# Performance work log

Measured on AMD Instinct MI355X. Metric: run time of the kernel, lower is better.

## Reference

```python
import jax, jax.numpy as jnp
import numpy as np

EMB = 512
HEADS = 8
B, T = 4, 1024


def setup_inputs() -> dict:
    key = jax.random.key(0)
    k1, k2, k3, k4, k5 = jax.random.split(key, 5)
    scale = 1.0 / np.sqrt(EMB)
    x = jax.random.normal(k1, (B, T, EMB), dtype=jnp.float32)
    # Linear(emb, emb*heads, bias=False) weights, stored as [in, out] for x @ W
    Wk = jax.random.normal(k2, (EMB, EMB * HEADS), dtype=jnp.float32) * scale
    Wq = jax.random.normal(k3, (EMB, EMB * HEADS), dtype=jnp.float32) * scale
    Wv = jax.random.normal(k4, (EMB, EMB * HEADS), dtype=jnp.float32) * scale
    Wu = jax.random.normal(k5, (EMB * HEADS, EMB), dtype=jnp.float32) * (1.0 / np.sqrt(EMB * HEADS))
    return {"x": x, "Wk": Wk, "Wq": Wq, "Wv": Wv, "Wu": Wu}


def reference(x, Wk, Wq, Wv, Wu):
    b, t, k = x.shape
    h = HEADS
    # projections -> [b, h, t, k]
    keys = (x @ Wk).reshape(b, t, h, k).transpose(0, 2, 1, 3)
    queries = (x @ Wq).reshape(b, t, h, k).transpose(0, 2, 1, 3)
    values = (x @ Wv).reshape(b, t, h, k).transpose(0, 2, 1, 3)
    # NOTE: original computes bmm(keys, queries^T): dot[i,j] = key_i . query_j
    dot = jnp.einsum('bhik,bhjk->bhij', keys, queries)  # [b,h,t,t]
    # mask_fn: only upper-triangle (offset=1) entries that are EXACTLY zero get -inf
    triu = jnp.triu(jnp.ones((t, t), dtype=bool), k=1)
    final_mask = triu & (dot == 0)
    dot = jnp.where(final_mask, -jnp.inf, dot)
    attn = jax.nn.softmax(dot, axis=-1)
    out = jnp.einsum('bhij,bhjk->bhik', attn, values)  # [b,h,t,k]
    out = out.transpose(0, 2, 1, 3).reshape(b, t, h * k)
    return out @ Wu
```

## Files before the change

### kernel.cpp

```cpp
#include <hip/hip_runtime.h>
#include <stdint.h>

typedef _Float16 f16x8 __attribute__((ext_vector_type(8)));
typedef float f32x4 __attribute__((ext_vector_type(4)));

__device__ __forceinline__ unsigned short f2h(float f) {
  _Float16 h = (_Float16)f;
  return __builtin_bit_cast(unsigned short, h);
}

#if __has_builtin(__builtin_amdgcn_global_load_lds)
#define HAVE_GLL 1
__device__ __forceinline__ void gload_lds16(const void* g, void* l) {
  auto gp = reinterpret_cast<const __attribute__((address_space(1))) void*>(
      reinterpret_cast<uintptr_t>(g));
  auto lp = reinterpret_cast<__attribute__((address_space(3))) void*>(
      reinterpret_cast<uintptr_t>(l));
  __builtin_amdgcn_global_load_lds(gp, lp, 16, 0, 0);
}
#else
#define HAVE_GLL 0
#endif

__device__ __forceinline__ void transpose_core(const float* in, unsigned short* out,
                                               int R, int C, int c0, int r0) {
  __shared__ float t[32][33];
  int tx = threadIdx.x & 31, ty = threadIdx.x >> 5;
#pragma unroll
  for (int i = 0; i < 32; i += 8)
    t[ty + i][tx] = in[(long)(r0 + ty + i) * C + (c0 + tx)];
  __syncthreads();
#pragma unroll
  for (int i = 0; i < 32; i += 8)
    out[(long)(c0 + ty + i) * R + (r0 + tx)] = f2h(t[tx][ty + i]);
}

__global__ __launch_bounds__(256) void k_setup(
    const float* __restrict__ x, const float* __restrict__ W0, const float* __restrict__ W1,
    const float* __restrict__ W2, const float* __restrict__ W3,
    unsigned short* __restrict__ Xh, unsigned short* __restrict__ o0,
    unsigned short* __restrict__ o1, unsigned short* __restrict__ o2,
    unsigned short* __restrict__ o3) {
  int z = blockIdx.z;
  if (z == 4) {
    int i = (blockIdx.y * 128 + blockIdx.x) * 256 + threadIdx.x;
    float4 v = reinterpret_cast<const float4*>(x)[i];
    ushort4 o;
    o.x = f2h(v.x); o.y = f2h(v.y); o.z = f2h(v.z); o.w = f2h(v.w);
    reinterpret_cast<ushort4*>(Xh)[i] = o;
  } else if (z < 3) {
    const float* in = (z == 0) ? W0 : (z == 1) ? W1 : W2;
    unsigned short* out = (z == 0) ? o0 : (z == 1) ? o1 : o2;
    transpose_core(in, out, 512, 4096, blockIdx.x * 32, blockIdx.y * 32);
  } else {
    transpose_core(W3, o3, 4096, 512, blockIdx.y * 32, blockIdx.x * 32);
  }
}

template <int OUT>
__device__ __forceinline__ void gemm_core(const unsigned short* __restrict__ A,
                                          const unsigned short* __restrict__ B,
                                          void* __restrict__ Cv, int K, int lda, int ldb,
                                          int ldc, long coff, int m0, int n0) {
  __shared__ unsigned short As[128 * 64];
  __shared__ unsigned short Bs[128 * 64];

  int tid = threadIdx.x;
  int wid = tid >> 6, lane = tid & 63;
  int wm = (wid >> 1) * 64, wn = (wid & 1) * 64;
  int rq = lane >> 4, rl = lane & 15;

  f32x4 acc[4][4];
#pragma unroll
  for (int i = 0; i < 4; ++i)
#pragma unroll
    for (int j = 0; j < 4; ++j) acc[i][j] = (f32x4){0.f, 0.f, 0.f, 0.f};

#if HAVE_GLL
  int cg = (lane & 7) ^ ((lane >> 3) & 7);
  int rl8 = lane >> 3;
#endif

  for (int k0 = 0; k0 < K; k0 += 64) {
    __syncthreads();
#if HAVE_GLL
#pragma unroll
    for (int t = 0; t < 4; ++t) {
      int r = wid * 32 + t * 8;
      gload_lds16(&A[(long)(m0 + r + rl8) * lda + k0 + cg * 8], &As[r * 64]);
      gload_lds16(&B[(long)(n0 + r + rl8) * ldb + k0 + cg * 8], &Bs[r * 64]);
    }
#else
#pragma unroll
    for (int it = 0; it < 4; ++it) {
      int idx = tid + it * 256;
      int r = idx >> 3, c = idx & 7;
      int cs = c ^ (r & 7);
      *reinterpret_cast<uint4*>(&As[r * 64 + cs * 8]) =
          *reinterpret_cast<const uint4*>(&A[(long)(m0 + r) * lda + k0 + c * 8]);
      *reinterpret_cast<uint4*>(&Bs[r * 64 + cs * 8]) =
          *reinterpret_cast<const uint4*>(&B[(long)(n0 + r) * ldb + k0 + c * 8]);
    }
#endif
    __syncthreads();
#pragma unroll
    for (int ks = 0; ks < 2; ++ks) {
      f16x8 af[4], bfr[4];
      int kc = ks * 4 + rq;
#pragma unroll
      for (int i = 0; i < 4; ++i) {
        int ra = wm + i * 16 + rl;
        af[i] = *reinterpret_cast<const f16x8*>(&As[ra * 64 + ((kc ^ (ra & 7)) << 3)]);
        int rb = wn + i * 16 + rl;
        bfr[i] = *reinterpret_cast<const f16x8*>(&Bs[rb * 64 + ((kc ^ (rb & 7)) << 3)]);
      }
#pragma unroll
      for (int i = 0; i < 4; ++i)
#pragma unroll
        for (int j = 0; j < 4; ++j)
          acc[i][j] = __builtin_amdgcn_mfma_f32_16x16x32_f16(af[i], bfr[j], acc[i][j], 0, 0, 0);
    }
  }

#pragma unroll
  for (int i = 0; i < 4; ++i)
#pragma unroll
    for (int j = 0; j < 4; ++j)
#pragma unroll
      for (int r = 0; r < 4; ++r) {
        long row = m0 + wm + i * 16 + rq * 4 + r;
        long col = n0 + wn + j * 16 + rl;
        float v = acc[i][j][r];
        if (OUT == 1)
          reinterpret_cast<unsigned short*>(Cv)[coff + row * ldc + col] = f2h(v);
        else if (OUT == 0)
          reinterpret_cast<float*>(Cv)[coff + row * ldc + col] = v;
        else
          atomicAdd(&reinterpret_cast<float*>(Cv)[coff + row * ldc + col], v);
      }
}

template <int OUT>
__global__ __launch_bounds__(256, 2) void k_gemm_btx(
    const unsigned short* __restrict__ A, const unsigned short* __restrict__ B,
    void* __restrict__ Cv, int K, int lda, int ldb, int ldc,
    long oAo, long oAi, long oBo, long oBi, long oCo, long oCi, int zdiv,
    int sx, int sy) {
  int c = blockIdx.x, w = blockIdx.y;
  int z = c + 8 * (w >> (sx + sy));
  int y = (w >> sx) & ((1 << sy) - 1);
  int x = w & ((1 << sx) - 1);
  A += (long)(z / zdiv) * oAo + (long)(z % zdiv) * oAi;
  B += (long)(z / zdiv) * oBo + (long)(z % zdiv) * oBi;
  long coff = (long)(z / zdiv) * oCo + (long)(z % zdiv) * oCi;
  gemm_core<OUT>(A, B, Cv, K, lda, ldb, ldc, coff, y * 128, x * 128);
}

__global__ __launch_bounds__(256, 2) void k_gemm_qkv(
    const unsigned short* __restrict__ X, const unsigned short* __restrict__ Wqt,
    const unsigned short* __restrict__ Wkt, const unsigned short* __restrict__ Wvt,
    unsigned short* __restrict__ Qb, unsigned short* __restrict__ Kb,
    unsigned short* __restrict__ Vt) {
  int z = blockIdx.z;
  const unsigned short* A = (z == 2) ? Wvt : X;
  const unsigned short* B = (z == 0) ? Wqt : (z == 1) ? Wkt : X;
  unsigned short* C = (z == 0) ? Qb : (z == 1) ? Kb : Vt;
  gemm_core<1>(A, B, C, 512, 512, 512, 4096, 0, blockIdx.y * 128, blockIdx.x * 128);
}

__global__ __launch_bounds__(256, 2) void k_gemm_splitk(
    const unsigned short* __restrict__ A, const unsigned short* __restrict__ B,
    float* __restrict__ C, int lda, int ldb, int ldc) {
  int c = blockIdx.x, w = blockIdx.y;
  int g = c + 8 * (w >> 2);
  int y = g & 31, z = g >> 5, x = w & 3;
  gemm_core<2>(A + (long)z * 1024, B + (long)z * 1024, C, 1024, lda, ldb, ldc, 0,
               y * 128, x * 128);
}

__global__ __launch_bounds__(256) void k_softmax_w(unsigned short* __restrict__ S) {
  long row = (long)blockIdx.x * 4 + (threadIdx.x >> 6);
  int lane = threadIdx.x & 63;
  f16x8* p = reinterpret_cast<f16x8*>(S + row * 1024);
  f16x8 a = p[lane * 2], b = p[lane * 2 + 1];
  float v[16];
#pragma unroll
  for (int i = 0; i < 8; ++i) { v[i] = (float)a[i]; v[8 + i] = (float)b[i]; }
  float m = v[0];
#pragma unroll
  for (int i = 1; i < 16; ++i) m = fmaxf(m, v[i]);
#pragma unroll
  for (int o = 32; o; o >>= 1) m = fmaxf(m, __shfl_xor(m, o));
  float s = 0.f;
#pragma unroll
  for (int i = 0; i < 16; ++i) { v[i] = __expf(v[i] - m); s += v[i]; }
#pragma unroll
  for (int o = 32; o; o >>= 1) s += __shfl_xor(s, o);
  float inv = 1.0f / s;
  f16x8 oa, ob;
#pragma unroll
  for (int i = 0; i < 8; ++i) {
    oa[i] = (_Float16)(v[i] * inv);
    ob[i] = (_Float16)(v[8 + i] * inv);
  }
  p[lane * 2] = oa;
  p[lane * 2 + 1] = ob;
}

__global__ void k_sentinel(float* out, float v) { out[0] = v; }

extern "C" void kernel_launch(void* const* d_in, const int* in_sizes, int n_in,
                              void* d_out, int out_size, void* d_ws, size_t ws_size,
                              hipStream_t stream) {
  const float* x  = (const float*)d_in[0];
  const float* Wk = (const float*)d_in[1];
  const float* Wq = (const float*)d_in[2];
  const float* Wv = (const float*)d_in[3];
  const float* Wu = (const float*)d_in[4];
  float* out = (float*)d_out;

  const long SZ_X = 4096L * 512;
  const long SZ_W = 512L * 4096;
  const size_t NEED = 188743680;

  if (ws_size < NEED) {
    hipMemsetAsync(d_out, 0, (size_t)out_size * 4, stream);
    k_sentinel<<<1, 1, 0, stream>>>(out, (float)ws_size);
    return;
  }

  char* p = (char*)d_ws;
  unsigned short* Xbf = (unsigned short*)p; p += SZ_X * 2;
  unsigned short* Wqt = (unsigned short*)p; p += SZ_W * 2;
  unsigned short* Wkt = (unsigned short*)p; p += SZ_W * 2;
  unsigned short* Wvt = (unsigned short*)p; p += SZ_W * 2;
  unsigned short* Wut = (unsigned short*)p; p += SZ_W * 2;
  unsigned short* Qb = (unsigned short*)p; p += 4096L * 4096 * 2;
  unsigned short* Kb = (unsigned short*)p; p += 4096L * 4096 * 2;
  unsigned short* Vt = (unsigned short*)p; p += 4096L * 4096 * 2;
  unsigned short* S16 = (unsigned short*)p;
  unsigned short* Ob = Qb;

  hipMemsetAsync(d_out, 0, (size_t)out_size * 4, stream);

  k_setup<<<dim3(128, 16, 5), 256, 0, stream>>>(x, Wq, Wk, Wv, Wu, Xbf, Wqt, Wkt, Wvt, Wut);

  k_gemm_qkv<<<dim3(32, 32, 3), 256, 0, stream>>>(Xbf, Wqt, Wkt, Wvt, Qb, Kb, Vt);

  k_gemm_btx<1><<<dim3(8, 256), 256, 0, stream>>>(
      Kb, Qb, S16, 512, 4096, 4096, 1024,
      4194304, 512, 4194304, 512, 8388608, 1048576, 8, 3, 3);
  k_softmax_w<<<8192, 256, 0, stream>>>(S16);
  k_gemm_btx<1><<<dim3(8, 128), 256, 0, stream>>>(
      S16, Vt, Ob, 1024, 1024, 4096, 4096,
      8388608, 1048576, 1024, 2097152, 4194304, 512, 8, 2, 3);

  k_gemm_splitk<<<dim3(8, 64), 256, 0, stream>>>(Ob, Wut, out, 4096, 4096, 512);
}
```

Baseline: 284.3 us.

## Fold Wv into Wu to fuse value and output projections

Precomputes per-head Wv·Wu products so values are projected directly into the output space, giving VU of width 512 per head. The PV matmul and the final output projection then collapse into a single split-K GEMM that accumulates atomically into the output. Scores are written in an interleaved layout so the new softmax and the fused GEMM can read P as one wide matrix. This removes the large [4096x4096] O intermediate and one GEMM, but adds a small weight-product GEMM, changes the fp16 rounding path, and relies on atomics across heads.

```diff
diff --git a/kernel.cpp b/kernel.cpp
--- a/kernel.cpp
+++ b/kernel.cpp
@@ -36,24 +36,26 @@
 }
 
 __global__ __launch_bounds__(256) void k_setup(
-    const float* __restrict__ x, const float* __restrict__ W0, const float* __restrict__ W1,
-    const float* __restrict__ W2, const float* __restrict__ W3,
-    unsigned short* __restrict__ Xh, unsigned short* __restrict__ o0,
-    unsigned short* __restrict__ o1, unsigned short* __restrict__ o2,
-    unsigned short* __restrict__ o3) {
+    const float* __restrict__ x, const float* __restrict__ Wq, const float* __restrict__ Wk,
+    const float* __restrict__ Wv, const float* __restrict__ Wu,
+    unsigned short* __restrict__ Xh, unsigned short* __restrict__ Wqt,
+    unsigned short* __restrict__ Wkt, unsigned short* __restrict__ Wvh,
+    unsigned short* __restrict__ Wut) {
   int z = blockIdx.z;
-  if (z == 4) {
+  if (z == 0) {
+    transpose_core(Wq, Wqt, 512, 4096, blockIdx.x * 32, blockIdx.y * 32);
+  } else if (z == 1) {
+    transpose_core(Wk, Wkt, 512, 4096, blockIdx.x * 32, blockIdx.y * 32);
+  } else if (z == 2) {
+    transpose_core(Wu, Wut, 4096, 512, blockIdx.y * 32, blockIdx.x * 32);
+  } else {
+    const float* in = (z == 3) ? x : Wv;
+    unsigned short* out = (z == 3) ? Xh : Wvh;
     int i = (blockIdx.y * 128 + blockIdx.x) * 256 + threadIdx.x;
-    float4 v = reinterpret_cast<const float4*>(x)[i];
+    float4 v = reinterpret_cast<const float4*>(in)[i];
     ushort4 o;
     o.x = f2h(v.x); o.y = f2h(v.y); o.z = f2h(v.z); o.w = f2h(v.w);
-    reinterpret_cast<ushort4*>(Xh)[i] = o;
-  } else if (z < 3) {
-    const float* in = (z == 0) ? W0 : (z == 1) ? W1 : W2;
-    unsigned short* out = (z == 0) ? o0 : (z == 1) ? o1 : o2;
-    transpose_core(in, out, 512, 4096, blockIdx.x * 32, blockIdx.y * 32);
-  } else {
-    transpose_core(W3, o3, 4096, 512, blockIdx.y * 32, blockIdx.x * 32);
+    reinterpret_cast<ushort4*>(out)[i] = o;
   }
 }
 
@@ -128,15 +130,20 @@
     for (int j = 0; j < 4; ++j)
 #pragma unroll
       for (int r = 0; r < 4; ++r) {
-        long row = m0 + wm + i * 16 + rq * 4 + r;
-        long col = n0 + wn + j * 16 + rl;
+        int row = m0 + wm + i * 16 + rq * 4 + r;
+        int col = n0 + wn + j * 16 + rl;
         float v = acc[i][j][r];
         if (OUT == 1)
-          reinterpret_cast<unsigned short*>(Cv)[coff + row * ldc + col] = f2h(v);
+          reinterpret_cast<unsigned short*>(Cv)[coff + (long)row * ldc + col] = f2h(v);
         else if (OUT == 0)
-          reinterpret_cast<float*>(Cv)[coff + row * ldc + col] = v;
-        else
-          atomicAdd(&reinterpret_cast<float*>(Cv)[coff + row * ldc + col], v);
+          reinterpret_cast<float*>(Cv)[coff + (long)row * ldc + col] = v;
+        else if (OUT == 2)
+          atomicAdd(&reinterpret_cast<float*>(Cv)[coff + (long)row * ldc + col], v);
+        else {
+          long addr = (long)(col >> 10) * 4194304 + (long)(row & 511) * 8192 +
+                      ((row >> 9) << 10) + (col & 1023);
+          reinterpret_cast<unsigned short*>(Cv)[addr] = f2h(v);
+        }
       }
 }
 
@@ -158,50 +165,48 @@
 
 __global__ __launch_bounds__(256, 2) void k_gemm_qkv(
     const unsigned short* __restrict__ X, const unsigned short* __restrict__ Wqt,
-    const unsigned short* __restrict__ Wkt, const unsigned short* __restrict__ Wvt,
+    const unsigned short* __restrict__ Wkt, const unsigned short* __restrict__ Wvut,
     unsigned short* __restrict__ Qb, unsigned short* __restrict__ Kb,
-    unsigned short* __restrict__ Vt) {
-  int z = blockIdx.z;
-  const unsigned short* A = (z == 2) ? Wvt : X;
-  const unsigned short* B = (z == 0) ? Wqt : (z == 1) ? Wkt : X;
-  unsigned short* C = (z == 0) ? Qb : (z == 1) ? Kb : Vt;
-  gemm_core<1>(A, B, C, 512, 512, 512, 4096, 0, blockIdx.y * 128, blockIdx.x * 128);
-}
-
-__global__ __launch_bounds__(256, 2) void k_gemm_splitk(
-    const unsigned short* __restrict__ A, const unsigned short* __restrict__ B,
-    float* __restrict__ C, int lda, int ldb, int ldc) {
+    unsigned short* __restrict__ VUb) {
   int c = blockIdx.x, w = blockIdx.y;
-  int g = c + 8 * (w >> 2);
-  int y = g & 31, z = g >> 5, x = w & 3;
-  gemm_core<2>(A + (long)z * 1024, B + (long)z * 1024, C, 1024, lda, ldb, ldc, 0,
-               y * 128, x * 128);
-}
-
-__global__ __launch_bounds__(256) void k_softmax_w(unsigned short* __restrict__ S) {
-  long row = (long)blockIdx.x * 4 + (threadIdx.x >> 6);
+  int z = w >> 7;
+  int r = w & 127;
+  if (z < 2) {
+    int x = 4 * c + (r & 3), y = r >> 2;
+    gemm_core<1>(X, (z == 0) ? Wqt : Wkt, (z == 0) ? Qb : Kb, 512, 512, 512, 4096, 0,
+                 y * 128, x * 128);
+  } else {
+    int y = 4 * c + (r & 3), x = r >> 2;
+    gemm_core<3>(Wvut, X, VUb, 512, 512, 512, 0, 0, y * 128, x * 128);
+  }
+}
+
+__global__ __launch_bounds__(256) void k_softmax_x(unsigned short* __restrict__ S) {
+  int g = blockIdx.y * 4 + (threadIdx.x >> 6);
+  int b = g >> 10, i = g & 1023;
+  long base = (long)b * 8388608 + (long)i * 8192 + (long)blockIdx.x * 1024;
   int lane = threadIdx.x & 63;
-  f16x8* p = reinterpret_cast<f16x8*>(S + row * 1024);
-  f16x8 a = p[lane * 2], b = p[lane * 2 + 1];
+  f16x8* p = reinterpret_cast<f16x8*>(S + base);
+  f16x8 a = p[lane * 2], bb = p[lane * 2 + 1];
   float v[16];
 #pragma unroll
-  for (int i = 0; i < 8; ++i) { v[i] = (float)a[i]; v[8 + i] = (float)b[i]; }
+  for (int q = 0; q < 8; ++q) { v[q] = (float)a[q]; v[8 + q] = (float)bb[q]; }
   float m = v[0];
 #pragma unroll
-  for (int i = 1; i < 16; ++i) m = fmaxf(m, v[i]);
+  for (int q = 1; q < 16; ++q) m = fmaxf(m, v[q]);
 #pragma unroll
   for (int o = 32; o; o >>= 1) m = fmaxf(m, __shfl_xor(m, o));
   float s = 0.f;
 #pragma unroll
-  for (int i = 0; i < 16; ++i) { v[i] = __expf(v[i] - m); s += v[i]; }
+  for (int q = 0; q < 16; ++q) { v[q] = __expf(v[q] - m); s += v[q]; }
 #pragma unroll
   for (int o = 32; o; o >>= 1) s += __shfl_xor(s, o);
   float inv = 1.0f / s;
   f16x8 oa, ob;
 #pragma unroll
-  for (int i = 0; i < 8; ++i) {
-    oa[i] = (_Float16)(v[i] * inv);
-    ob[i] = (_Float16)(v[8 + i] * inv);
+  for (int q = 0; q < 8; ++q) {
+    oa[q] = (_Float16)(v[q] * inv);
+    ob[q] = (_Float16)(v[8 + q] * inv);
   }
   p[lane * 2] = oa;
   p[lane * 2 + 1] = ob;
@@ -230,30 +235,34 @@
   }
 
   char* p = (char*)d_ws;
-  unsigned short* Xbf = (unsigned short*)p; p += SZ_X * 2;
-  unsigned short* Wqt = (unsigned short*)p; p += SZ_W * 2;
-  unsigned short* Wkt = (unsigned short*)p; p += SZ_W * 2;
-  unsigned short* Wvt = (unsigned short*)p; p += SZ_W * 2;
-  unsigned short* Wut = (unsigned short*)p; p += SZ_W * 2;
-  unsigned short* Qb = (unsigned short*)p; p += 4096L * 4096 * 2;
-  unsigned short* Kb = (unsigned short*)p; p += 4096L * 4096 * 2;
-  unsigned short* Vt = (unsigned short*)p; p += 4096L * 4096 * 2;
-  unsigned short* S16 = (unsigned short*)p;
-  unsigned short* Ob = Qb;
+  unsigned short* Xbf  = (unsigned short*)p; p += SZ_X * 2;
+  unsigned short* Wqt  = (unsigned short*)p; p += SZ_W * 2;
+  unsigned short* Wkt  = (unsigned short*)p; p += SZ_W * 2;
+  unsigned short* Wut  = (unsigned short*)p; p += SZ_W * 2;
+  unsigned short* Wvut = (unsigned short*)p; p += SZ_W * 2;
+  unsigned short* Qb   = (unsigned short*)p; p += 4096L * 4096 * 2;
+  unsigned short* Kb   = (unsigned short*)p; p += 4096L * 4096 * 2;
+  unsigned short* Pb   = (unsigned short*)p; p += 4096L * 8192 * 2;
+  unsigned short* VUb  = (unsigned short*)p;
+  unsigned short* Wvh  = VUb;
 
   hipMemsetAsync(d_out, 0, (size_t)out_size * 4, stream);
 
-  k_setup<<<dim3(128, 16, 5), 256, 0, stream>>>(x, Wq, Wk, Wv, Wu, Xbf, Wqt, Wkt, Wvt, Wut);
-
-  k_gemm_qkv<<<dim3(32, 32, 3), 256, 0, stream>>>(Xbf, Wqt, Wkt, Wvt, Qb, Kb, Vt);
+  k_setup<<<dim3(128, 16, 5), 256, 0, stream>>>(x, Wq, Wk, Wv, Wu, Xbf, Wqt, Wkt, Wvh, Wut);
+
+  k_gemm_btx<1><<<dim3(8, 16), 256, 0, stream>>>(
+      Wut, Wvh, Wvut, 512, 4096, 4096, 512,
+      512, 0, 512, 0, 262144, 0, 1, 2, 2);
+
+  k_gemm_qkv<<<dim3(8, 384), 256, 0, stream>>>(Xbf, Wqt, Wkt, Wvut, Qb, Kb, VUb);
 
   k_gemm_btx<1><<<dim3(8, 256), 256, 0, stream>>>(
-      Kb, Qb, S16, 512, 4096, 4096, 1024,
-      4194304, 512, 4194304, 512, 8388608, 1048576, 8, 3, 3);
-  k_softmax_w<<<8192, 256, 0, stream>>>(S16);
-  k_gemm_btx<1><<<dim3(8, 128), 256, 0, stream>>>(
-      S16, Vt, Ob, 1024, 1024, 4096, 4096,
-      8388608, 1048576, 1024, 2097152, 4194304, 512, 8, 2, 3);
-
-  k_gemm_splitk<<<dim3(8, 64), 256, 0, stream>>>(Ob, Wut, out, 4096, 4096, 512);
-}
+      Kb, Qb, Pb, 512, 4096, 4096, 8192,
+      4194304, 512, 4194304, 512, 8388608, 1024, 8, 3, 3);
+
+  k_softmax_x<<<dim3(8, 1024), 256, 0, stream>>>(Pb);
+
+  k_gemm_btx<2><<<dim3(8, 64), 256, 0, stream>>>(
+      Pb, VUb, out, 2048, 8192, 8192, 512,
+      8388608, 2048, 4194304, 2048, 524288, 0, 4, 2, 3);
+}
```

After: 297.4 us. 1.05x slower.
